# Kernel tuning notes

Measured on AMD Instinct MI355X. Metric: run time of the kernel, lower is better.

The kernel has to match this reference:

```python
import jax, jax.numpy as jnp
import numpy as np

N_COMPONENTS = 8
N_DIMENSIONS = 16
N_POINTS = 500000


def setup_inputs() -> dict:
    key = jax.random.key(0)
    k1, k2, k3 = jax.random.split(key, 3)
    data = jax.random.normal(k1, (N_POINTS, N_DIMENSIONS), dtype=jnp.float32)
    logits = jnp.ones((N_COMPONENTS,), dtype=jnp.float32)
    means = jax.random.normal(k2, (N_COMPONENTS, N_DIMENSIONS), dtype=jnp.float32)
    scales = jax.random.normal(k3, (N_COMPONENTS, N_DIMENSIONS, N_DIMENSIONS), dtype=jnp.float32)
    return {"data": data, "logits": logits, "means": means, "scales": scales}


def _gmm_log_prob(data, logits, means, scales):
    # covariances = scales @ scales^T  -> [K, D, D]
    covs = jnp.einsum('kij,klj->kil', scales, scales)
    L = jnp.linalg.cholesky(covs)  # [K, D, D]
    # diff: [K, N, D]
    diff = data[None, :, :] - means[:, None, :]
    # solve L y = diff^T  -> y: [K, D, N]
    y = jax.scipy.linalg.solve_triangular(L, jnp.swapaxes(diff, 1, 2), lower=True)
    maha = jnp.sum(y * y, axis=1)  # [K, N]
    half_logdet = jnp.sum(jnp.log(jnp.diagonal(L, axis1=1, axis2=2)), axis=-1)  # [K]
    D = data.shape[-1]
    log2pi = jnp.float32(np.log(2.0 * np.pi))
    comp_lp = -0.5 * (maha + D * log2pi) - half_logdet[:, None]  # [K, N]
    mix_lp = jax.nn.log_softmax(logits)  # [K]
    return jax.scipy.special.logsumexp(mix_lp[:, None] + comp_lp, axis=0)  # [N]


def reference(data, logits, means, scales):
    return _gmm_log_prob(data, logits, means, scales)
```

## Files before the change

kernel.cpp:

```cpp
#include <hip/hip_runtime.h>
#include <math.h>

#define KC 8
#define DD 16
#define BLK 256

__global__ __launch_bounds__(128) void gmm_prep(
    const float* __restrict__ logits,
    const float* __restrict__ means,
    const float* __restrict__ scales,
    float* __restrict__ Aout,
    float* __restrict__ Bout,
    float* __restrict__ Cout)
{
    const int tid  = threadIdx.x;
    const int k    = tid >> 4;
    const int i    = tid & 15;
    const int lane = tid & 63;
    const int base = lane & 48;

    float srow[DD];
    {
        const float4* sp = (const float4*)(scales + (size_t)(k * DD + i) * DD);
#pragma unroll
        for (int q = 0; q < 4; ++q) {
            float4 v = sp[q];
            srow[4 * q + 0] = v.x; srow[4 * q + 1] = v.y;
            srow[4 * q + 2] = v.z; srow[4 * q + 3] = v.w;
        }
    }

    float a[DD];
#pragma unroll
    for (int j = 0; j < DD; ++j) a[j] = 0.f;
#pragma unroll
    for (int d = 0; d < DD; ++d) {
        float sid = srow[d];
#pragma unroll
        for (int j = 0; j < DD; ++j) {
            float sjd = __shfl(srow[d], base + j, 64);
            a[j] = fmaf(sid, sjd, a[j]);
        }
    }

    float l[DD];
    float hld = 0.f;
#pragma unroll
    for (int j = 0; j < DD; ++j) {
        float ajj = __shfl(a[j], base + j, 64);
        float ljj = sqrtf(ajj);
        hld += logf(ljj);
        float lij = (i < j) ? 0.f : (a[j] / ljj);
        l[j] = lij;
#pragma unroll
        for (int c = j + 1; c < DD; ++c) {
            float lcj = __shfl(l[j], base + c, 64);
            a[c] = fmaf(-lij, lcj, a[c]);
        }
    }

    float xc[DD];
#pragma unroll
    for (int r = 0; r < DD; ++r) {
        float s = (r == i) ? 1.f : 0.f;
#pragma unroll
        for (int t = 0; t < DD; ++t) {
            if (t < r) {
                float lrt = __shfl(l[t], base + r, 64);
                s = fmaf(-lrt, xc[t], s);
            }
        }
        float lrr = __shfl(l[r], base + r, 64);
        xc[r] = (r < i) ? 0.f : (s / lrr);
    }

    __shared__ float Ash[KC][DD][DD + 1];
#pragma unroll
    for (int r = 0; r < DD; ++r) Ash[k][r][i] = xc[r];
    __syncthreads();

    float bb = 0.f;
#pragma unroll
    for (int j = 0; j < DD; ++j) {
        float aij = Ash[k][i][j];
        Aout[(k * DD + i) * DD + j] = aij;
        bb = fmaf(aij, means[k * DD + j], bb);
    }
    Bout[k * DD + i] = bb;

    if (i == 0) {
        float mx = logits[0];
        for (int t = 1; t < KC; ++t) mx = fmaxf(mx, logits[t]);
        float se = 0.f;
        for (int t = 0; t < KC; ++t) se += expf(logits[t] - mx);
        float lse = mx + logf(se);
        const float log2pi = 1.8378770664093453f;
        Cout[k] = (logits[k] - lse) - hld - 0.5f * DD * log2pi;
    }
}

__global__ __launch_bounds__(BLK, 6) void gmm_lp(
    const float* __restrict__ data,
    const float* __restrict__ Ag,
    const float* __restrict__ Bg,
    const float* __restrict__ Cg,
    float* __restrict__ out, int N)
{
    const int id = blockIdx.x * BLK + threadIdx.x;
    const int cl = id < N ? id : N - 1;

    float x[DD];
    {
        const float4* xp = (const float4*)(data + (size_t)cl * DD);
#pragma unroll
        for (int q = 0; q < 4; ++q) {
            float4 v = xp[q];
            x[4 * q + 0] = v.x; x[4 * q + 1] = v.y;
            x[4 * q + 2] = v.z; x[4 * q + 3] = v.w;
        }
    }

    float mx = -1e30f, sum = 0.f;

#pragma unroll 1
    for (int k = 0; k < KC; ++k) {
        const float* Ak = Ag + k * DD * DD;
        float bk[DD];
        {
            const float4* b4 = (const float4*)(Bg + k * DD);
#pragma unroll
            for (int q = 0; q < 4; ++q) {
                float4 v = b4[q];
                bk[4 * q + 0] = v.x; bk[4 * q + 1] = v.y;
                bk[4 * q + 2] = v.z; bk[4 * q + 3] = v.w;
            }
        }
        const float ck = Cg[k];

        float maha = 0.f;
#pragma unroll
        for (int i = 0; i < DD; ++i) {
            float y = -bk[i];
#pragma unroll
            for (int g = 0; g <= i / 4; ++g) {
                float4 a = *(const float4*)(Ak + i * DD + 4 * g);
                y = fmaf(a.x, x[4 * g + 0], y);
                y = fmaf(a.y, x[4 * g + 1], y);
                y = fmaf(a.z, x[4 * g + 2], y);
                y = fmaf(a.w, x[4 * g + 3], y);
            }
            maha = fmaf(y, y, maha);
        }

        float lpk = fmaf(-0.5f, maha, ck);
        float nm = fmaxf(mx, lpk);
        sum = sum * __expf(mx - nm) + __expf(lpk - nm);
        mx = nm;
    }

    if (id < N) out[id] = mx + __logf(sum);
}

extern "C" void kernel_launch(void* const* d_in, const int* in_sizes, int n_in,
                              void* d_out, int out_size, void* d_ws, size_t ws_size,
                              hipStream_t stream) {
    const float* data   = (const float*)d_in[0];
    const float* logits = (const float*)d_in[1];
    const float* means  = (const float*)d_in[2];
    const float* scales = (const float*)d_in[3];
    float* out = (float*)d_out;
    const int N = in_sizes[0] / DD;

    float* A = (float*)d_ws;
    float* B = A + KC * DD * DD;
    float* C = B + KC * DD;

    gmm_prep<<<1, 128, 0, stream>>>(logits, means, scales, A, B, C);
    const int nblk = (N + BLK - 1) / BLK;
    gmm_lp<<<nblk, BLK, 0, stream>>>(data, A, B, C, out, N);
}
```

Before: 105.5 us.

## Compute Mahalanobis projections with split-bf16 MFMA instead of scalar FMAs

Reformulates the per-component triangular matrix-vector product as 16x16x32 bf16 MFMA operations. Both the precomputed inverse-Cholesky matrix (with the mean offset folded in as an extra column) and the data points are split into high and low bf16 parts, and three MFMAs per tile approximate fp32 precision. Data points are staged through LDS to form the B operand, and squared norms are reduced across lanes with shuffles. This moves most of the arithmetic from VALU to the matrix cores, at the cost of bf16x3 precision loss, LDS traffic, and lower occupancy (launch bound of 4 blocks instead of 6).

```diff
diff --git a/kernel.cpp b/kernel.cpp
--- a/kernel.cpp
+++ b/kernel.cpp
@@ -4,13 +4,21 @@
 #define KC 8
 #define DD 16
 #define BLK 256
+
+typedef short short8 __attribute__((ext_vector_type(8)));
+typedef float floatx4 __attribute__((ext_vector_type(4)));
+
+__device__ __forceinline__ unsigned bf16h(float x) {
+    unsigned u = __float_as_uint(x);
+    return (u + 0x7FFFu + ((u >> 16) & 1u)) & 0xFFFF0000u;
+}
 
 __global__ __launch_bounds__(128) void gmm_prep(
     const float* __restrict__ logits,
     const float* __restrict__ means,
     const float* __restrict__ scales,
-    float* __restrict__ Aout,
-    float* __restrict__ Bout,
+    uint4* __restrict__ AH,
+    uint4* __restrict__ AL,
     float* __restrict__ Cout)
 {
     const int tid  = threadIdx.x;
@@ -79,14 +87,34 @@
     for (int r = 0; r < DD; ++r) Ash[k][r][i] = xc[r];
     __syncthreads();
 
+    float rowv[32];
     float bb = 0.f;
 #pragma unroll
     for (int j = 0; j < DD; ++j) {
         float aij = Ash[k][i][j];
-        Aout[(k * DD + i) * DD + j] = aij;
+        rowv[j] = aij;
         bb = fmaf(aij, means[k * DD + j], bb);
     }
-    Bout[k * DD + i] = bb;
+    rowv[16] = -bb;
+#pragma unroll
+    for (int j = 17; j < 32; ++j) rowv[j] = 0.f;
+
+#pragma unroll
+    for (int q = 0; q < 4; ++q) {
+        unsigned dh[4], dl[4];
+#pragma unroll
+        for (int jj = 0; jj < 4; ++jj) {
+            float e = rowv[q * 8 + 2 * jj];
+            float o = rowv[q * 8 + 2 * jj + 1];
+            unsigned he = bf16h(e), ho = bf16h(o);
+            float re = e - __uint_as_float(he);
+            float ro = o - __uint_as_float(ho);
+            dh[jj] = ho | (he >> 16);
+            dl[jj] = bf16h(ro) | (bf16h(re) >> 16);
+        }
+        AH[k * 64 + q * 16 + i] = make_uint4(dh[0], dh[1], dh[2], dh[3]);
+        AL[k * 64 + q * 16 + i] = make_uint4(dl[0], dl[1], dl[2], dl[3]);
+    }
 
     if (i == 0) {
         float mx = logits[0];
@@ -99,15 +127,20 @@
     }
 }
 
-__global__ __launch_bounds__(BLK, 6) void gmm_lp(
+__global__ __launch_bounds__(BLK, 4) void gmm_lp(
     const float* __restrict__ data,
-    const float* __restrict__ Ag,
-    const float* __restrict__ Bg,
+    const uint4* __restrict__ AH,
+    const uint4* __restrict__ AL,
     const float* __restrict__ Cg,
     float* __restrict__ out, int N)
 {
-    const int id = blockIdx.x * BLK + threadIdx.x;
-    const int cl = id < N ? id : N - 1;
+    __shared__ unsigned lds[4 * 1536];
+
+    const int tid  = threadIdx.x;
+    const int lane = tid & 63;
+    const int wv   = tid >> 6;
+    const int id   = blockIdx.x * BLK + tid;
+    const int cl   = id < N ? id : N - 1;
 
     float x[DD];
     {
@@ -120,39 +153,77 @@
         }
     }
 
+    unsigned dh[8], dl[8];
+#pragma unroll
+    for (int jj = 0; jj < 8; ++jj) {
+        float e = x[2 * jj], o = x[2 * jj + 1];
+        unsigned he = bf16h(e), ho = bf16h(o);
+        float re = e - __uint_as_float(he);
+        float ro = o - __uint_as_float(ho);
+        dh[jj] = ho | (he >> 16);
+        dl[jj] = bf16h(ro) | (bf16h(re) >> 16);
+    }
+
+    const int wb = wv * 1536 + lane * 12;
+    *(uint4*)&lds[wb + 0] = make_uint4(dh[0], dh[1], dh[2], dh[3]);
+    *(uint4*)&lds[wb + 4] = make_uint4(dh[4], dh[5], dh[6], dh[7]);
+    *(uint4*)&lds[wb + 768 + 0] = make_uint4(dl[0], dl[1], dl[2], dl[3]);
+    *(uint4*)&lds[wb + 768 + 4] = make_uint4(dl[4], dl[5], dl[6], dl[7]);
+
+    const int q = lane >> 4, c = lane & 15;
+    short8 bh[4], bl[4];
+#pragma unroll
+    for (int t = 0; t < 4; ++t) {
+        uint4 uh, ul;
+        if (q < 2) {
+            int ad = wv * 1536 + (16 * t + c) * 12 + q * 4;
+            uh = *(const uint4*)&lds[ad];
+            ul = *(const uint4*)&lds[ad + 768];
+        } else if (q == 2) {
+            uh = make_uint4(0x00003F80u, 0u, 0u, 0u);
+            ul = make_uint4(0u, 0u, 0u, 0u);
+        } else {
+            uh = make_uint4(0u, 0u, 0u, 0u);
+            ul = make_uint4(0u, 0u, 0u, 0u);
+        }
+        bh[t] = __builtin_bit_cast(short8, uh);
+        bl[t] = __builtin_bit_cast(short8, ul);
+    }
+
     float mx = -1e30f, sum = 0.f;
 
 #pragma unroll 1
     for (int k = 0; k < KC; ++k) {
-        const float* Ak = Ag + k * DD * DD;
-        float bk[DD];
-        {
-            const float4* b4 = (const float4*)(Bg + k * DD);
-#pragma unroll
-            for (int q = 0; q < 4; ++q) {
-                float4 v = b4[q];
-                bk[4 * q + 0] = v.x; bk[4 * q + 1] = v.y;
-                bk[4 * q + 2] = v.z; bk[4 * q + 3] = v.w;
-            }
-        }
-        const float ck = Cg[k];
-
-        float maha = 0.f;
-#pragma unroll
-        for (int i = 0; i < DD; ++i) {
-            float y = -bk[i];
-#pragma unroll
-            for (int g = 0; g <= i / 4; ++g) {
-                float4 a = *(const float4*)(Ak + i * DD + 4 * g);
-                y = fmaf(a.x, x[4 * g + 0], y);
-                y = fmaf(a.y, x[4 * g + 1], y);
-                y = fmaf(a.z, x[4 * g + 2], y);
-                y = fmaf(a.w, x[4 * g + 3], y);
-            }
-            maha = fmaf(y, y, maha);
-        }
-
-        float lpk = fmaf(-0.5f, maha, ck);
+        short8 ah = __builtin_bit_cast(short8, AH[k * 64 + lane]);
+        short8 al = __builtin_bit_cast(short8, AL[k * 64 + lane]);
+        float ck = Cg[k];
+
+        floatx4 acc[4];
+#pragma unroll
+        for (int t = 0; t < 4; ++t) {
+            floatx4 z = {0.f, 0.f, 0.f, 0.f};
+            floatx4 a0 = __builtin_amdgcn_mfma_f32_16x16x32_bf16(ah, bh[t], z, 0, 0, 0);
+            a0 = __builtin_amdgcn_mfma_f32_16x16x32_bf16(ah, bl[t], a0, 0, 0, 0);
+            a0 = __builtin_amdgcn_mfma_f32_16x16x32_bf16(al, bh[t], a0, 0, 0, 0);
+            acc[t] = a0;
+        }
+
+        float s[4];
+#pragma unroll
+        for (int t = 0; t < 4; ++t) {
+            float v = acc[t][0] * acc[t][0];
+            v = fmaf(acc[t][1], acc[t][1], v);
+            v = fmaf(acc[t][2], acc[t][2], v);
+            v = fmaf(acc[t][3], acc[t][3], v);
+            v += __shfl_xor(v, 16, 64);
+            v += __shfl_xor(v, 32, 64);
+            s[t] = v;
+        }
+        float m01 = (q & 1) ? s[1] : s[0];
+        float m23 = (q & 1) ? s[3] : s[2];
+        float mm  = (q & 2) ? m23 : m01;
+
+        float lpk = fmaf(-0.5f, mm, ck);
         float nm = fmaxf(mx, lpk);
         sum = sum * __expf(mx - nm) + __expf(lpk - nm);
         mx = nm;
@@ -171,11 +242,11 @@
     float* out = (float*)d_out;
     const int N = in_sizes[0] / DD;
 
-    float* A = (float*)d_ws;
-    float* B = A + KC * DD * DD;
-    float* C = B + KC * DD;
-
-    gmm_prep<<<1, 128, 0, stream>>>(logits, means, scales, A, B, C);
+    uint4* AH = (uint4*)d_ws;
+    uint4* AL = AH + KC * 64;
+    float* C  = (float*)(AL + KC * 64);
+
+    gmm_prep<<<1, 128, 0, stream>>>(logits, means, scales, AH, AL, C);
     const int nblk = (N + BLK - 1) / BLK;
-    gmm_lp<<<nblk, BLK, 0, stream>>>(data, A, B, C, out, N);
-}
+    gmm_lp<<<nblk, BLK, 0, stream>>>(data, AH, AL, C, out, N);
+}
```

Result: faster. 96.51 us (-8.6%).

## Compute Mahalanobis transforms with split-bf16 MFMA instead of scalar FMAs

Applied to the files above, without the earlier changes.

Replaces the per-thread scalar triangular matrix-vector product with 32x32x16 bf16 MFMA operations. The fp32 inverse-Cholesky factors and data points are each split into hi/lo bf16 parts, and three MFMAs (hi*hi, hi*lo, lo*hi) recover near-fp32 accuracy. Two components are packed per MFMA tile, with the bias preloaded into the accumulator. The aim is to move the dominant FMA work onto matrix cores. In exchange it adds packing overhead, cross-half shuffles, a lower occupancy hint, and a small precision loss from dropping the lo*lo term.

```diff
diff --git a/kernel.cpp b/kernel.cpp
--- a/kernel.cpp
+++ b/kernel.cpp
@@ -4,13 +4,19 @@
 #define KC 8
 #define DD 16
 #define BLK 256
+
+typedef short short8 __attribute__((ext_vector_type(8)));
+typedef float floatx16 __attribute__((ext_vector_type(16)));
+
+__device__ __forceinline__ unsigned asu(float x) { return __float_as_uint(x); }
 
 __global__ __launch_bounds__(128) void gmm_prep(
     const float* __restrict__ logits,
     const float* __restrict__ means,
     const float* __restrict__ scales,
-    float* __restrict__ Aout,
-    float* __restrict__ Bout,
+    uint4* __restrict__ AH2,
+    uint4* __restrict__ AL2,
+    float* __restrict__ BF,
     float* __restrict__ Cout)
 {
     const int tid  = threadIdx.x;
@@ -79,14 +85,39 @@
     for (int r = 0; r < DD; ++r) Ash[k][r][i] = xc[r];
     __syncthreads();
 
+    float rowA[DD];
     float bb = 0.f;
 #pragma unroll
     for (int j = 0; j < DD; ++j) {
         float aij = Ash[k][i][j];
-        Aout[(k * DD + i) * DD + j] = aij;
+        rowA[j] = aij;
         bb = fmaf(aij, means[k * DD + j], bb);
     }
-    Bout[k * DD + i] = bb;
+
+    const int P = k >> 1;
+    const int m = (k & 1) * 16 + i;
+#pragma unroll
+    for (int h = 0; h < 2; ++h) {
+        unsigned dh[4], dl[4];
+#pragma unroll
+        for (int jj = 0; jj < 4; ++jj) {
+            float e = rowA[h * 8 + 2 * jj];
+            float o = rowA[h * 8 + 2 * jj + 1];
+            unsigned he = asu(e) & 0xFFFF0000u, ho = asu(o) & 0xFFFF0000u;
+            float re = e - __uint_as_float(he);
+            float ro = o - __uint_as_float(ho);
+            dh[jj] = (he >> 16) | ho;
+            dl[jj] = ((asu(re) & 0xFFFF0000u) >> 16) | (asu(ro) & 0xFFFF0000u);
+        }
+        AH2[P * 64 + h * 32 + m] = make_uint4(dh[0], dh[1], dh[2], dh[3]);
+        AL2[P * 64 + h * 32 + m] = make_uint4(dl[0], dl[1], dl[2], dl[3]);
+    }
+
+    {
+        const int h = (m >> 2) & 1;
+        const int t = (m & 3) | ((m >> 3) << 2);
+        BF[P * 32 + h * 16 + t] = -bb;
+    }
 
     if (i == 0) {
         float mx = logits[0];
@@ -99,65 +130,84 @@
     }
 }
 
-__global__ __launch_bounds__(BLK, 6) void gmm_lp(
+__global__ __launch_bounds__(BLK, 4) void gmm_lp(
     const float* __restrict__ data,
-    const float* __restrict__ Ag,
-    const float* __restrict__ Bg,
+    const uint4* __restrict__ AH2,
+    const uint4* __restrict__ AL2,
+    const float* __restrict__ BF,
     const float* __restrict__ Cg,
     float* __restrict__ out, int N)
 {
-    const int id = blockIdx.x * BLK + threadIdx.x;
-    const int cl = id < N ? id : N - 1;
-
-    float x[DD];
-    {
-        const float4* xp = (const float4*)(data + (size_t)cl * DD);
-#pragma unroll
-        for (int q = 0; q < 4; ++q) {
-            float4 v = xp[q];
-            x[4 * q + 0] = v.x; x[4 * q + 1] = v.y;
-            x[4 * q + 2] = v.z; x[4 * q + 3] = v.w;
-        }
+    const int tid  = threadIdx.x;
+    const int lane = tid & 63;
+    const int half = lane >> 5;
+    const int wbase = blockIdx.x * BLK + (tid & ~63);
+
+    short8 bh[2], bl[2];
+#pragma unroll
+    for (int s = 0; s < 2; ++s) {
+        int p = wbase + s * 32 + (lane & 31);
+        p = p < N ? p : N - 1;
+        const float4* xp = (const float4*)(data + (size_t)p * DD + half * 8);
+        float4 v0 = xp[0], v1 = xp[1];
+        float xs[8] = {v0.x, v0.y, v0.z, v0.w, v1.x, v1.y, v1.z, v1.w};
+        unsigned dh[4], dl[4];
+#pragma unroll
+        for (int jj = 0; jj < 4; ++jj) {
+            float e = xs[2 * jj], o = xs[2 * jj + 1];
+            unsigned he = asu(e) & 0xFFFF0000u, ho = asu(o) & 0xFFFF0000u;
+            float re = e - __uint_as_float(he);
+            float ro = o - __uint_as_float(ho);
+            dh[jj] = __builtin_amdgcn_perm(ho, he, 0x07060302u);
+            dl[jj] = __builtin_amdgcn_perm(asu(ro), asu(re), 0x07060302u);
+        }
+        bh[s] = __builtin_bit_cast(short8, make_uint4(dh[0], dh[1], dh[2], dh[3]));
+        bl[s] = __builtin_bit_cast(short8, make_uint4(dl[0], dl[1], dl[2], dl[3]));
     }
 
     float mx = -1e30f, sum = 0.f;
 
 #pragma unroll 1
-    for (int k = 0; k < KC; ++k) {
-        const float* Ak = Ag + k * DD * DD;
-        float bk[DD];
-        {
-            const float4* b4 = (const float4*)(Bg + k * DD);
-#pragma unroll
-            for (int q = 0; q < 4; ++q) {
-                float4 v = b4[q];
-                bk[4 * q + 0] = v.x; bk[4 * q + 1] = v.y;
-                bk[4 * q + 2] = v.z; bk[4 * q + 3] = v.w;
+    for (int P = 0; P < 4; ++P) {
+        short8 ah = __builtin_bit_cast(short8, AH2[P * 64 + lane]);
+        short8 al = __builtin_bit_cast(short8, AL2[P * 64 + lane]);
+        const float4* bfp = (const float4*)(BF + P * 32 + half * 16);
+        float4 b0 = bfp[0], b1 = bfp[1], b2 = bfp[2], b3 = bfp[3];
+        float ck0 = Cg[2 * P], ck1 = Cg[2 * P + 1];
+
+        float me[2], mo[2];
+#pragma unroll
+        for (int s = 0; s < 2; ++s) {
+            floatx16 acc = {b0.x, b0.y, b0.z, b0.w, b1.x, b1.y, b1.z, b1.w,
+                            b2.x, b2.y, b2.z, b2.w, b3.x, b3.y, b3.z, b3.w};
+            acc = __builtin_amdgcn_mfma_f32_32x32x16_bf16(ah, bh[s], acc, 0, 0, 0);
+            acc = __builtin_amdgcn_mfma_f32_32x32x16_bf16(ah, bl[s], acc, 0, 0, 0);
+            acc = __builtin_amdgcn_mfma_f32_32x32x16_bf16(al, bh[s], acc, 0, 0, 0);
+            float se = acc[0] * acc[0], so = acc[8] * acc[8];
+#pragma unroll
+            for (int t = 1; t < 8; ++t) {
+                se = fmaf(acc[t], acc[t], se);
+                so = fmaf(acc[t + 8], acc[t + 8], so);
             }
-        }
-        const float ck = Cg[k];
-
-        float maha = 0.f;
-#pragma unroll
-        for (int i = 0; i < DD; ++i) {
-            float y = -bk[i];
-#pragma unroll
-            for (int g = 0; g <= i / 4; ++g) {
-                float4 a = *(const float4*)(Ak + i * DD + 4 * g);
-                y = fmaf(a.x, x[4 * g + 0], y);
-                y = fmaf(a.y, x[4 * g + 1], y);
-                y = fmaf(a.z, x[4 * g + 2], y);
-                y = fmaf(a.w, x[4 * g + 3], y);
-            }
-            maha = fmaf(y, y, maha);
-        }
-
-        float lpk = fmaf(-0.5f, maha, ck);
+            me[s] = se + __shfl_xor(se, 32, 64);
+            mo[s] = so + __shfl_xor(so, 32, 64);
+        }
+
+        float mE = half ? me[1] : me[0];
+        float mO = half ? mo[1] : mo[0];
+
+        float lpk = fmaf(-0.5f, mE, ck0);
         float nm = fmaxf(mx, lpk);
         sum = sum * __expf(mx - nm) + __expf(lpk - nm);
         mx = nm;
-    }
-
+
+        lpk = fmaf(-0.5f, mO, ck1);
+        nm = fmaxf(mx, lpk);
+        sum = sum * __expf(mx - nm) + __expf(lpk - nm);
+        mx = nm;
+    }
+
+    const int id = wbase + lane;
     if (id < N) out[id] = mx + __logf(sum);
 }
 
@@ -171,11 +221,12 @@
     float* out = (float*)d_out;
     const int N = in_sizes[0] / DD;
 
-    float* A = (float*)d_ws;
-    float* B = A + KC * DD * DD;
-    float* C = B + KC * DD;
-
-    gmm_prep<<<1, 128, 0, stream>>>(logits, means, scales, A, B, C);
+    uint4* AH2 = (uint4*)d_ws;
+    uint4* AL2 = AH2 + 4 * 64;
+    float* BF  = (float*)(AL2 + 4 * 64);
+    float* C   = BF + 128;
+
+    gmm_prep<<<1, 128, 0, stream>>>(logits, means, scales, AH2, AL2, BF, C);
     const int nblk = (N + BLK - 1) / BLK;
-    gmm_lp<<<nblk, BLK, 0, stream>>>(data, A, B, C, out, N);
+    gmm_lp<<<nblk, BLK, 0, stream>>>(data, AH2, AL2, BF, C, out, N);
 }
```

After: 92.33 us. 1.14x faster.
